# Performance work log

Measured on AMD Instinct MI355X. Metric: run time of the kernel, lower is better.

Reference implementation:

```python
import jax, jax.numpy as jnp
import numpy as np

B = 16384
IN = 512
A = 16
E = 9  # 9 position-specific experts
H1, H2, H3 = 512, 256, 128


def setup_inputs() -> dict:
    key = jax.random.key(0)
    ks = jax.random.split(key, 10)
    s = lambda fan_in: 1.0 / np.sqrt(fan_in)
    return {
        "x": jax.random.normal(ks[0], (B, IN), dtype=jnp.float32),
        "position": jax.random.randint(ks[1], (B,), 0, 9, dtype=jnp.int64),
        # torch Linear convention: W [out, in], y = x @ W.T + b; stacked per expert [E, out, in]
        "W1": jax.random.uniform(ks[2], (E, H1, IN), jnp.float32, -s(IN), s(IN)),
        "b1": jax.random.uniform(ks[3], (E, H1), jnp.float32, -s(IN), s(IN)),
        "W2": jax.random.uniform(ks[4], (E, H2, H1), jnp.float32, -s(H1), s(H1)),
        "b2": jax.random.uniform(ks[5], (E, H2), jnp.float32, -s(H1), s(H1)),
        "W3": jax.random.uniform(ks[6], (E, H3, H2), jnp.float32, -s(H2), s(H2)),
        "b3": jax.random.uniform(ks[7], (E, H3), jnp.float32, -s(H2), s(H2)),
        "W4": jax.random.uniform(ks[8], (E, A, H3), jnp.float32, -s(H3), s(H3)),
        "b4": jax.random.uniform(ks[9], (E, A), jnp.float32, -s(H3), s(H3)),
    }


def reference(x, position, W1, b1, W2, b2, W3, b3, W4, b4):
    # Each sample i is routed through expert min(position[i], 8).
    # Dense MoE reference: run all 9 experts over the full batch, then
    # select the routed expert's logits per sample (same math as the
    # per-sample Python loop in the original module).
    pos = jnp.minimum(position, 8)
    h = jax.nn.relu(jnp.einsum('bi,eoi->ebo', x, W1) + b1[:, None, :])   # [E,B,H1]
    h = jax.nn.relu(jnp.einsum('ebi,eoi->ebo', h, W2) + b2[:, None, :])  # [E,B,H2]
    h = jax.nn.relu(jnp.einsum('ebi,eoi->ebo', h, W3) + b3[:, None, :])  # [E,B,H3]
    logits_all = jnp.einsum('ebi,eoi->ebo', h, W4) + b4[:, None, :]      # [E,B,A]
    logits = logits_all[pos, jnp.arange(x.shape[0])]                     # [B,A]
    return jax.nn.softmax(logits, axis=1)
```

## Files before the change

kernel.cpp:

```cpp
#include <hip/hip_runtime.h>

typedef _Float16 f16;
typedef __attribute__((ext_vector_type(8))) _Float16 f16x8;
typedef __attribute__((ext_vector_type(4))) _Float16 f16x4;
typedef __attribute__((ext_vector_type(4))) float f32x4;

#define MFMA16(a, b, c) __builtin_amdgcn_mfma_f32_16x16x32_f16(a, b, c, 0, 0, 0)

#define B_N 16384
#define E_N 9
#define TILE 48
#define NT_GRID 352
#define THREADS 512

#define D_IN 512
#define D_H1 512
#define D_H2 256
#define D_H3 128
#define D_A 16

#define RPW 104
#define O4B 7667712
#define WPL_BYTES 7704576
#define WSLOTS (WPL_BYTES / 16)

#define IDX_OFF 64
#define WP_OFF 131584
#define WS_NEED (WP_OFF + (size_t)WPL_BYTES)

#define H2_OFF 49152
#define LDS_BYTES 73728


__global__ void k_bucket(const int* __restrict__ pos, int* __restrict__ hdr,
                         int* __restrict__ idx) {
  __shared__ int cnt[E_N], cur[E_N];
  __shared__ int flag_s;
  const int t = threadIdx.x;
  if (t < E_N) cnt[t] = 0;
  if (t == 0) {
    int nz = 0;
    for (int i = 0; i < 64; ++i) nz |= pos[2 * i + 1];
    flag_s = (nz == 0) ? 1 : 0;
  }
  __syncthreads();
  const bool f64 = flag_s != 0;
  int e[16];
#pragma unroll
  for (int k = 0; k < 16; ++k) {
    int i = k * 1024 + t;
    long long v = f64 ? ((const long long*)pos)[i] : (long long)pos[i];
    v = v < 0 ? 0 : (v > 8 ? 8 : v);
    e[k] = (int)v;
    atomicAdd(&cnt[e[k]], 1);
  }
  __syncthreads();
  if (t == 0) {
    int acc = 0;
    for (int ee = 0; ee < E_N; ++ee) { cur[ee] = acc; acc += cnt[ee]; }
  }
  if (t < E_N) hdr[8 + t] = cnt[t];
  __syncthreads();
#pragma unroll
  for (int k = 0; k < 16; ++k) {
    int i = k * 1024 + t;
    int slot = atomicAdd(&cur[e[k]], 1);
    idx[slot] = i;
  }
}


__global__ void k_wcvt(const float* __restrict__ W1, const float* __restrict__ W2,
                       const float* __restrict__ W3, const float* __restrict__ W4,
                       char* __restrict__ wp) {
  int slot = blockIdx.x * 256 + threadIdx.x;
  if (slot >= WSLOTS) return;
  long addr = (long)slot << 4;
  int lane = slot & 63;
  int lg = lane >> 4, ln = lane & 15;
  const float* src;
  if (addr < O4B) {
    int rec = (int)(addr >> 10);
    int f = rec % RPW;
    int ew = rec / RPW;
    int w = ew & 7, e = ew >> 3;
    if (f < 64) {
      int kk = f >> 2, nf = f & 3;
      int n = w * 64 + nf * 16 + ln;
      int k = kk * 32 + lg * 8;
      src = W1 + ((long)e * D_H1 + n) * D_IN + k;
    } else if (f < 96) {
      int j = f - 64;
      int kk = j >> 1, nf = j & 1;
      int n = w * 32 + nf * 16 + ln;
      int k = kk * 32 + lg * 8;
      src = W2 + ((long)e * D_H2 + n) * D_H1 + k;
    } else {
      int kk = f - 96;
      int n = w * 16 + ln;
      int k = kk * 32 + lg * 8;
      src = W3 + ((long)e * D_H3 + n) * D_H2 + k;
    }
  } else {
    long rel = addr - O4B;
    int e = (int)(rel >> 12);
    int r2 = (int)(rel & 4095);
    int s = r2 >> 4, n = s >> 4, k16 = s & 15;
    src = W4 + ((long)e * D_A + n) * D_H3 + k16 * 8;
  }
  float4 a = *(const float4*)src;
  float4 b = *(const float4*)(src + 4);
  f16x8 h;
  h[0] = (f16)a.x; h[1] = (f16)a.y; h[2] = (f16)a.z; h[3] = (f16)a.w;
  h[4] = (f16)b.x; h[5] = (f16)b.y; h[6] = (f16)b.z; h[7] = (f16)b.w;
  *(f16x8*)(wp + addr) = h;
}


__device__ __forceinline__ f16x8 afrag(const char* base, int strideB, int rowoff,
                                       int kbytes, int lane) {
  int m = rowoff + (lane & 15);
  int q = kbytes + ((lane >> 4) * 16);
  return *(const f16x8*)(base + m * strideB + (q ^ ((m & 15) << 4)));
}

__device__ __forceinline__ f16x8 ldfrag(const char* wb, int f, int lane) {
  return *(const f16x8*)(wb + (long)f * 1024 + lane * 16);
}

__launch_bounds__(THREADS, 2)
__global__ void k_mlp(const float* __restrict__ x,
                      const float* __restrict__ b1, const float* __restrict__ b2,
                      const float* __restrict__ b3, const float* __restrict__ b4,
                      const int* __restrict__ hdr, const int* __restrict__ idx,
                      const char* __restrict__ wp, float* __restrict__ out) {
  __shared__ __align__(16) char lds[LDS_BYTES];

  int b = blockIdx.x;
  int bswz = (b & 7) * (NT_GRID / 8) + (b >> 3);

  const int* counts = hdr + 8;
  int e = -1, tile = 0, base = 0, ne = 0;
  {
    int acc = 0, off = 0;
    for (int ee = 0; ee < E_N; ++ee) {
      int n = counts[ee];
      int nt = (n + TILE - 1) / TILE;
      if (bswz < acc + nt) { e = ee; tile = bswz - acc; ne = n; base = off; break; }
      acc += nt; off += n;
    }
  }
  if (e < 0) return;
  const int rvalid = min(TILE, ne - tile * TILE);
  const int row0 = base + tile * TILE;

  const int t = threadIdx.x;
  const int lane = t & 63;
  const int wid = t >> 6;
  const int lg = lane >> 4;
  const int ln = lane & 15;

  const char* wb = wp + ((long)(e * 8 + wid) * RPW << 10);
  const char* wpe4 = wp + O4B + (long)e * 4096;

  f16x8 Q[8];
#pragma unroll
  for (int i = 0; i < 8; ++i) Q[i] = ldfrag(wb, i, lane);

  const float4* x4 = (const float4*)x;
#pragma unroll
  for (int v8 = 0; v8 < 12; ++v8) {
    int u = v8 * THREADS + t;
    int s = u >> 7, c4 = u & 127;
    float4 v = make_float4(0.f, 0.f, 0.f, 0.f);
    if (s < rvalid) v = x4[(long)idx[row0 + s] * (D_IN / 4) + c4];
    f16x4 h;
    h[0] = (f16)v.x; h[1] = (f16)v.y; h[2] = (f16)v.z; h[3] = (f16)v.w;
    *(f16x4*)(lds + s * 1024 + ((c4 * 8) ^ ((s & 15) << 4))) = h;
  }
  __syncthreads();

  {
    f32x4 acc1[3][4];
#pragma unroll
    for (int m = 0; m < 3; ++m)
#pragma unroll
      for (int r = 0; r < 4; ++r) acc1[m][r] = (f32x4){0.f, 0.f, 0.f, 0.f};

#pragma unroll
    for (int ss = 0; ss < 16; ++ss) {
      f16x8 A0 = afrag(lds, 1024, 0, ss * 64, lane);
      f16x8 A1 = afrag(lds, 1024, 16, ss * 64, lane);
      f16x8 A2 = afrag(lds, 1024, 32, ss * 64, lane);
      __builtin_amdgcn_s_setprio(1);
#pragma unroll
      for (int r = 0; r < 4; ++r) {
        const int i = ss * 4 + r;
        acc1[0][r] = MFMA16(A0, Q[i & 7], acc1[0][r]);
        acc1[1][r] = MFMA16(A1, Q[i & 7], acc1[1][r]);
        acc1[2][r] = MFMA16(A2, Q[i & 7], acc1[2][r]);
        Q[i & 7] = ldfrag(wb, i + 8, lane);
      }
      __builtin_amdgcn_s_setprio(0);
      __builtin_amdgcn_sched_barrier(0);
    }
    __syncthreads();

#pragma unroll
    for (int nf = 0; nf < 4; ++nf) {
      int n = wid * 64 + nf * 16 + ln;
      float bias = b1[e * D_H1 + n];
#pragma unroll
      for (int m = 0; m < 3; ++m)
#pragma unroll
        for (int j = 0; j < 4; ++j) {
          float v = acc1[m][nf][j] + bias;
          v = v > 0.f ? v : 0.f;
          int rw = m * 16 + lg * 4 + j;
          *(f16*)(lds + rw * 1024 + ((n * 2) ^ ((rw & 15) << 4))) = (f16)v;
        }
    }
  }
  __syncthreads();

  {
    f32x4 acc2[3][2];
#pragma unroll
    for (int m = 0; m < 3; ++m)
#pragma unroll
      for (int nf = 0; nf < 2; ++nf) acc2[m][nf] = (f32x4){0.f, 0.f, 0.f, 0.f};

#pragma unroll
    for (int ss = 16; ss < 24; ++ss) {
#pragma unroll
      for (int hh = 0; hh < 2; ++hh) {
        const int kk = (ss - 16) * 2 + hh;
        f16x8 A0 = afrag(lds, 1024, 0, kk * 64, lane);
        f16x8 A1 = afrag(lds, 1024, 16, kk * 64, lane);
        f16x8 A2 = afrag(lds, 1024, 32, kk * 64, lane);
        __builtin_amdgcn_s_setprio(1);
#pragma unroll
        for (int nf = 0; nf < 2; ++nf) {
          const int i = ss * 4 + hh * 2 + nf;
          acc2[0][nf] = MFMA16(A0, Q[i & 7], acc2[0][nf]);
          acc2[1][nf] = MFMA16(A1, Q[i & 7], acc2[1][nf]);
          acc2[2][nf] = MFMA16(A2, Q[i & 7], acc2[2][nf]);
          if (i < 96) Q[i & 7] = ldfrag(wb, i + 8, lane);
        }
        __builtin_amdgcn_s_setprio(0);
      }
      __builtin_amdgcn_sched_barrier(0);
    }
#pragma unroll
    for (int nf = 0; nf < 2; ++nf) {
      int n = wid * 32 + nf * 16 + ln;
      float bias = b2[e * D_H2 + n];
#pragma unroll
      for (int m = 0; m < 3; ++m)
#pragma unroll
        for (int j = 0; j < 4; ++j) {
          float v = acc2[m][nf][j] + bias;
          v = v > 0.f ? v : 0.f;
          int rw = m * 16 + lg * 4 + j;
          *(f16*)(lds + H2_OFF + rw * 512 + ((n * 2) ^ ((rw & 15) << 4))) = (f16)v;
        }
    }
  }
  __syncthreads();

  {
    f32x4 acc3[3];
#pragma unroll
    for (int m = 0; m < 3; ++m) acc3[m] = (f32x4){0.f, 0.f, 0.f, 0.f};
    __builtin_amdgcn_s_setprio(1);
#pragma unroll
    for (int kk = 0; kk < 8; ++kk) {
      const int i = 96 + kk;
      f16x8 A0 = afrag(lds + H2_OFF, 512, 0, kk * 64, lane);
      f16x8 A1 = afrag(lds + H2_OFF, 512, 16, kk * 64, lane);
      f16x8 A2 = afrag(lds + H2_OFF, 512, 32, kk * 64, lane);
      acc3[0] = MFMA16(A0, Q[i & 7], acc3[0]);
      acc3[1] = MFMA16(A1, Q[i & 7], acc3[1]);
      acc3[2] = MFMA16(A2, Q[i & 7], acc3[2]);
    }
    __builtin_amdgcn_s_setprio(0);
    int n = wid * 16 + ln;
    float bias = b3[e * D_H3 + n];
#pragma unroll
    for (int m = 0; m < 3; ++m)
#pragma unroll
      for (int j = 0; j < 4; ++j) {
        float v = acc3[m][j] + bias;
        v = v > 0.f ? v : 0.f;
        int rw = m * 16 + lg * 4 + j;
        *(f16*)(lds + rw * 256 + ((n * 2) ^ ((rw & 15) << 4))) = (f16)v;
      }
  }
  __syncthreads();

  if (wid < 3) {
    f32x4 a4 = (f32x4){0.f, 0.f, 0.f, 0.f};
#pragma unroll
    for (int kc = 0; kc < 4; ++kc) {
      f16x8 Bv = *(const f16x8*)(wpe4 + ln * 256 + kc * 64 + lg * 16);
      f16x8 Av = afrag(lds, 256, wid * 16, kc * 64, lane);
      a4 = MFMA16(Av, Bv, a4);
    }
    float bias = b4[e * D_A + ln];
#pragma unroll
    for (int j = 0; j < 4; ++j) {
      float v = a4[j] + bias;
      float mx = v;
      for (int msk = 8; msk >= 1; msk >>= 1) mx = fmaxf(mx, __shfl_xor(mx, msk));
      float pe = expf(v - mx);
      float sm = pe;
      for (int msk = 8; msk >= 1; msk >>= 1) sm += __shfl_xor(sm, msk);
      int rl = wid * 16 + lg * 4 + j;
      if (rl < rvalid) out[(long)idx[row0 + rl] * D_A + ln] = pe / sm;
    }
  }
}


extern "C" void kernel_launch(void* const* d_in, const int* in_sizes, int n_in,
                              void* d_out, int out_size, void* d_ws, size_t ws_size,
                              hipStream_t stream) {
  const float* x  = (const float*)d_in[0];
  const int* pos  = (const int*)d_in[1];
  const float* W1 = (const float*)d_in[2];
  const float* b1 = (const float*)d_in[3];
  const float* W2 = (const float*)d_in[4];
  const float* b2 = (const float*)d_in[5];
  const float* W3 = (const float*)d_in[6];
  const float* b3 = (const float*)d_in[7];
  const float* W4 = (const float*)d_in[8];
  const float* b4 = (const float*)d_in[9];
  float* out = (float*)d_out;

  int* hdr = (int*)d_ws;
  int* idx = hdr + IDX_OFF;
  char* wp = (char*)d_ws + WP_OFF;

  hipLaunchKernelGGL(k_bucket, dim3(1), dim3(1024), 0, stream, pos, hdr, idx);
  hipLaunchKernelGGL(k_wcvt, dim3(WSLOTS / 256), dim3(256), 0, stream,
                     W1, W2, W3, W4, wp);
  hipLaunchKernelGGL(k_mlp, dim3(NT_GRID), dim3(THREADS), 0, stream,
                     x, b1, b2, b3, b4, hdr, idx, wp, out);
}
```

Baseline: 68.84 us.

## Stream weight fragments through an LDS ring via async global_load_lds and shrink tile

Replaces the per-wave register prefetch queue of weight fragments with a 3-slot LDS ring filled by global_load_lds DMA, synchronised with explicit vmcnt waits. The row tile shrinks from 48 to 32 and the grid grows to 520 blocks, so more blocks share the work and fewer registers are held per wave. The aim is to free VGPRs and overlap weight streaming with MFMA work. In exchange each weight fragment is now fetched by more tiles in total, and every step adds an LDS round-trip plus a wait.

```diff
diff --git a/kernel.cpp b/kernel.cpp
--- a/kernel.cpp
+++ b/kernel.cpp
@@ -9,8 +9,8 @@
 
 #define B_N 16384
 #define E_N 9
-#define TILE 48
-#define NT_GRID 352
+#define TILE 32
+#define NTILE_MAX 520
 #define THREADS 512
 
 #define D_IN 512
@@ -26,9 +26,9 @@
 
 #define IDX_OFF 64
 #define WP_OFF 131584
-#define WS_NEED (WP_OFF + (size_t)WPL_BYTES)
-
-#define H2_OFF 49152
+
+#define H2_OFF 32768
+#define RING_OFF 49152
 #define LDS_BYTES 73728
 
 
@@ -124,8 +124,21 @@
   return *(const f16x8*)(base + m * strideB + (q ^ ((m & 15) << 4)));
 }
 
-__device__ __forceinline__ f16x8 ldfrag(const char* wb, int f, int lane) {
-  return *(const f16x8*)(wb + (long)f * 1024 + lane * 16);
+__device__ __forceinline__ void dma16(const char* g, char* l) {
+  __builtin_amdgcn_global_load_lds(
+      (const __attribute__((address_space(1))) void*)g,
+      (__attribute__((address_space(3))) void*)l, 16, 0, 0);
+}
+
+template <int N> __device__ __forceinline__ void waitv();
+template <> __device__ __forceinline__ void waitv<2>() {
+  asm volatile("s_waitcnt vmcnt(2)" ::: "memory");
+}
+template <> __device__ __forceinline__ void waitv<1>() {
+  asm volatile("s_waitcnt vmcnt(1)" ::: "memory");
+}
+template <> __device__ __forceinline__ void waitv<0>() {
+  asm volatile("s_waitcnt vmcnt(0)" ::: "memory");
 }
 
 __launch_bounds__(THREADS, 2)
@@ -137,7 +150,7 @@
   __shared__ __align__(16) char lds[LDS_BYTES];
 
   int b = blockIdx.x;
-  int bswz = (b & 7) * (NT_GRID / 8) + (b >> 3);
+  int bswz = (b & 7) * (NTILE_MAX / 8) + (b >> 3);
 
   const int* counts = hdr + 8;
   int e = -1, tile = 0, base = 0, ne = 0;
@@ -162,14 +175,15 @@
 
   const char* wb = wp + ((long)(e * 8 + wid) * RPW << 10);
   const char* wpe4 = wp + O4B + (long)e * 4096;
-
-  f16x8 Q[8];
-#pragma unroll
-  for (int i = 0; i < 8; ++i) Q[i] = ldfrag(wb, i, lane);
+  char* ringw = lds + RING_OFF + wid * 3072;
+
+  dma16(wb + 0 * 1024 + lane * 16, ringw + 0 * 1024);
+  dma16(wb + 1 * 1024 + lane * 16, ringw + 1 * 1024);
+  dma16(wb + 2 * 1024 + lane * 16, ringw + 2 * 1024);
 
   const float4* x4 = (const float4*)x;
 #pragma unroll
-  for (int v8 = 0; v8 < 12; ++v8) {
+  for (int v8 = 0; v8 < 8; ++v8) {
     int u = v8 * THREADS + t;
     int s = u >> 7, c4 = u & 127;
     float4 v = make_float4(0.f, 0.f, 0.f, 0.f);
@@ -181,28 +195,28 @@
   __syncthreads();
 
   {
-    f32x4 acc1[3][4];
-#pragma unroll
-    for (int m = 0; m < 3; ++m)
-#pragma unroll
-      for (int r = 0; r < 4; ++r) acc1[m][r] = (f32x4){0.f, 0.f, 0.f, 0.f};
-
-#pragma unroll
-    for (int ss = 0; ss < 16; ++ss) {
-      f16x8 A0 = afrag(lds, 1024, 0, ss * 64, lane);
-      f16x8 A1 = afrag(lds, 1024, 16, ss * 64, lane);
-      f16x8 A2 = afrag(lds, 1024, 32, ss * 64, lane);
-      __builtin_amdgcn_s_setprio(1);
-#pragma unroll
-      for (int r = 0; r < 4; ++r) {
-        const int i = ss * 4 + r;
-        acc1[0][r] = MFMA16(A0, Q[i & 7], acc1[0][r]);
-        acc1[1][r] = MFMA16(A1, Q[i & 7], acc1[1][r]);
-        acc1[2][r] = MFMA16(A2, Q[i & 7], acc1[2][r]);
-        Q[i & 7] = ldfrag(wb, i + 8, lane);
+    f32x4 acc[2][4];
+#pragma unroll
+    for (int m = 0; m < 2; ++m)
+#pragma unroll
+      for (int nf = 0; nf < 4; ++nf) acc[m][nf] = (f32x4){0.f, 0.f, 0.f, 0.f};
+
+#pragma unroll
+    for (int kk = 0; kk < 16; ++kk) {
+      f16x8 A0 = afrag(lds, 1024, 0, kk * 64, lane);
+      f16x8 A1 = afrag(lds, 1024, 16, kk * 64, lane);
+#pragma unroll
+      for (int nf = 0; nf < 4; ++nf) {
+        const int rec = kk * 4 + nf;
+        waitv<2>();
+        f16x8 B = *(const f16x8*)(ringw + (rec % 3) * 1024 + lane * 16);
+        __builtin_amdgcn_s_setprio(1);
+        acc[0][nf] = MFMA16(A0, B, acc[0][nf]);
+        acc[1][nf] = MFMA16(A1, B, acc[1][nf]);
+        __builtin_amdgcn_s_setprio(0);
+        const int nr = rec + 3;
+        dma16(wb + (long)nr * 1024 + lane * 16, ringw + (nr % 3) * 1024);
       }
-      __builtin_amdgcn_s_setprio(0);
-      __builtin_amdgcn_sched_barrier(0);
     }
     __syncthreads();
 
@@ -211,10 +225,10 @@
       int n = wid * 64 + nf * 16 + ln;
       float bias = b1[e * D_H1 + n];
 #pragma unroll
-      for (int m = 0; m < 3; ++m)
+      for (int m = 0; m < 2; ++m)
 #pragma unroll
         for (int j = 0; j < 4; ++j) {
-          float v = acc1[m][nf][j] + bias;
+          float v = acc[m][nf][j] + bias;
           v = v > 0.f ? v : 0.f;
           int rw = m * 16 + lg * 4 + j;
           *(f16*)(lds + rw * 1024 + ((n * 2) ^ ((rw & 15) << 4))) = (f16)v;
@@ -224,39 +238,35 @@
   __syncthreads();
 
   {
-    f32x4 acc2[3][2];
-#pragma unroll
-    for (int m = 0; m < 3; ++m)
+    f32x4 acc2[2][2];
+#pragma unroll
+    for (int m = 0; m < 2; ++m)
 #pragma unroll
       for (int nf = 0; nf < 2; ++nf) acc2[m][nf] = (f32x4){0.f, 0.f, 0.f, 0.f};
 
 #pragma unroll
-    for (int ss = 16; ss < 24; ++ss) {
-#pragma unroll
-      for (int hh = 0; hh < 2; ++hh) {
-        const int kk = (ss - 16) * 2 + hh;
-        f16x8 A0 = afrag(lds, 1024, 0, kk * 64, lane);
-        f16x8 A1 = afrag(lds, 1024, 16, kk * 64, lane);
-        f16x8 A2 = afrag(lds, 1024, 32, kk * 64, lane);
+    for (int kk = 0; kk < 16; ++kk) {
+      f16x8 A0 = afrag(lds, 1024, 0, kk * 64, lane);
+      f16x8 A1 = afrag(lds, 1024, 16, kk * 64, lane);
+#pragma unroll
+      for (int nf = 0; nf < 2; ++nf) {
+        const int rec = 64 + kk * 2 + nf;
+        waitv<2>();
+        f16x8 B = *(const f16x8*)(ringw + (rec % 3) * 1024 + lane * 16);
         __builtin_amdgcn_s_setprio(1);
-#pragma unroll
-        for (int nf = 0; nf < 2; ++nf) {
-          const int i = ss * 4 + hh * 2 + nf;
-          acc2[0][nf] = MFMA16(A0, Q[i & 7], acc2[0][nf]);
-          acc2[1][nf] = MFMA16(A1, Q[i & 7], acc2[1][nf]);
-          acc2[2][nf] = MFMA16(A2, Q[i & 7], acc2[2][nf]);
-          if (i < 96) Q[i & 7] = ldfrag(wb, i + 8, lane);
-        }
+        acc2[0][nf] = MFMA16(A0, B, acc2[0][nf]);
+        acc2[1][nf] = MFMA16(A1, B, acc2[1][nf]);
         __builtin_amdgcn_s_setprio(0);
+        const int nr = rec + 3;
+        dma16(wb + (long)nr * 1024 + lane * 16, ringw + (nr % 3) * 1024);
       }
-      __builtin_amdgcn_sched_barrier(0);
     }
 #pragma unroll
     for (int nf = 0; nf < 2; ++nf) {
       int n = wid * 32 + nf * 16 + ln;
       float bias = b2[e * D_H2 + n];
 #pragma unroll
-      for (int m = 0; m < 3; ++m)
+      for (int m = 0; m < 2; ++m)
 #pragma unroll
         for (int j = 0; j < 4; ++j) {
           float v = acc2[m][nf][j] + bias;
@@ -269,25 +279,40 @@
   __syncthreads();
 
   {
-    f32x4 acc3[3];
-#pragma unroll
-    for (int m = 0; m < 3; ++m) acc3[m] = (f32x4){0.f, 0.f, 0.f, 0.f};
-    __builtin_amdgcn_s_setprio(1);
-#pragma unroll
-    for (int kk = 0; kk < 8; ++kk) {
-      const int i = 96 + kk;
-      f16x8 A0 = afrag(lds + H2_OFF, 512, 0, kk * 64, lane);
-      f16x8 A1 = afrag(lds + H2_OFF, 512, 16, kk * 64, lane);
-      f16x8 A2 = afrag(lds + H2_OFF, 512, 32, kk * 64, lane);
-      acc3[0] = MFMA16(A0, Q[i & 7], acc3[0]);
-      acc3[1] = MFMA16(A1, Q[i & 7], acc3[1]);
-      acc3[2] = MFMA16(A2, Q[i & 7], acc3[2]);
-    }
-    __builtin_amdgcn_s_setprio(0);
+    f32x4 acc3[2];
+    acc3[0] = (f32x4){0.f, 0.f, 0.f, 0.f};
+    acc3[1] = (f32x4){0.f, 0.f, 0.f, 0.f};
+
+#define L3STEP(REC, WAITN)                                                     \
+  {                                                                            \
+    const int kk3 = (REC) - 96;                                                \
+    f16x8 A0 = afrag(lds + H2_OFF, 512, 0, kk3 * 64, lane);                    \
+    f16x8 A1 = afrag(lds + H2_OFF, 512, 16, kk3 * 64, lane);                   \
+    waitv<WAITN>();                                                            \
+    f16x8 B = *(const f16x8*)(ringw + ((REC) % 3) * 1024 + lane * 16);         \
+    __builtin_amdgcn_s_setprio(1);                                             \
+    acc3[0] = MFMA16(A0, B, acc3[0]);                                          \
+    acc3[1] = MFMA16(A1, B, acc3[1]);                                          \
+    __builtin_amdgcn_s_setprio(0);                                             \
+    if ((REC) + 3 <= 103)                                                      \
+      dma16(wb + (long)((REC) + 3) * 1024 + lane * 16,                         \
+            ringw + (((REC) + 3) % 3) * 1024);                                 \
+  }
+
+    L3STEP(96, 2)
+    L3STEP(97, 2)
+    L3STEP(98, 2)
+    L3STEP(99, 2)
+    L3STEP(100, 2)
+    L3STEP(101, 2)
+    L3STEP(102, 1)
+    L3STEP(103, 0)
+#undef L3STEP
+
     int n = wid * 16 + ln;
     float bias = b3[e * D_H3 + n];
 #pragma unroll
-    for (int m = 0; m < 3; ++m)
+    for (int m = 0; m < 2; ++m)
 #pragma unroll
       for (int j = 0; j < 4; ++j) {
         float v = acc3[m][j] + bias;
@@ -298,7 +323,7 @@
   }
   __syncthreads();
 
-  if (wid < 3) {
+  if (wid < 2) {
     f32x4 a4 = (f32x4){0.f, 0.f, 0.f, 0.f};
 #pragma unroll
     for (int kc = 0; kc < 4; ++kc) {
@@ -344,6 +369,6 @@
   hipLaunchKernelGGL(k_bucket, dim3(1), dim3(1024), 0, stream, pos, hdr, idx);
   hipLaunchKernelGGL(k_wcvt, dim3(WSLOTS / 256), dim3(256), 0, stream,
                      W1, W2, W3, W4, wp);
-  hipLaunchKernelGGL(k_mlp, dim3(NT_GRID), dim3(THREADS), 0, stream,
+  hipLaunchKernelGGL(k_mlp, dim3(NTILE_MAX), dim3(THREADS), 0, stream,
                      x, b1, b2, b3, b4, hdr, idx, wp, out);
 }
```

Result: no change. 67.94 us (-1.3%).
